# Optimization experiments

Hardware: AMD Instinct MI355X
Metric: run time of the kernel (lower is better)

## Reference

```python
import jax, jax.numpy as jnp
import numpy as np

VOXEL_SIZE = np.array([0.2, 0.2, 4.0], dtype=np.float32)
PC_MIN = np.array([0.0, -40.0, -3.0], dtype=np.float32)
BN_EPS = 1e-3
N_POINTS = 1_500_000
N_VOXELS = 200_000
C_IN = 7   # (4 - 3) + 6 stats channels (cluster offset + voxel-center offset)
C_OUT = 64


def setup_inputs() -> dict:
    key = jax.random.key(0)
    ks = jax.random.split(key, 8)
    features = jax.random.normal(ks[0], (N_POINTS, 4), dtype=jnp.float32)
    point2voxel = jax.random.randint(ks[1], (N_POINTS,), 0, N_VOXELS).astype(jnp.int32)
    voxel_coors = jnp.stack([
        jax.random.randint(ks[2], (N_VOXELS,), 0, 2),    # batch idx
        jnp.zeros((N_VOXELS,), jnp.int32),               # z (pillars -> 0)
        jax.random.randint(ks[3], (N_VOXELS,), 0, 400),  # y bin
        jax.random.randint(ks[4], (N_VOXELS,), 0, 352),  # x bin
    ], axis=1).astype(jnp.int32)
    W = jax.random.normal(ks[5], (C_IN, C_OUT), dtype=jnp.float32) * 0.1
    bn_gamma = jnp.ones((C_OUT,), jnp.float32)
    bn_beta = jnp.zeros((C_OUT,), jnp.float32)
    bn_mean = jax.random.normal(ks[6], (C_OUT,), dtype=jnp.float32) * 0.01
    bn_var = jax.random.uniform(ks[7], (C_OUT,), minval=0.5, maxval=1.5, dtype=jnp.float32)
    return dict(features=features, W=W, bn_gamma=bn_gamma, bn_beta=bn_beta,
                bn_mean=bn_mean, bn_var=bn_var, point2voxel=point2voxel,
                voxel_coors=voxel_coors)


def reference(features, W, bn_gamma, bn_beta, bn_mean, bn_var, point2voxel, voxel_coors):
    M = voxel_coors.shape[0]
    xyz = features[:, :3]

    # --- stats: cluster-center offset (per-voxel mean of xyz, mapped back) ---
    cnt = jax.ops.segment_sum(jnp.ones((xyz.shape[0],), xyz.dtype), point2voxel,
                              num_segments=M)
    vmean = jax.ops.segment_sum(xyz, point2voxel, num_segments=M)
    vmean = vmean / jnp.maximum(cnt, 1.0)[:, None]
    cluster_off = xyz - vmean[point2voxel]

    # --- stats: voxel-center offset ---
    vs = jnp.asarray(VOXEL_SIZE)
    mn = jnp.asarray(PC_MIN)
    # coors layout is (batch, z, y, x) -> take (x, y, z)
    centers = (voxel_coors[:, jnp.array([3, 2, 1])].astype(jnp.float32) + 0.5) * vs + mn
    center_off = xyz - centers[point2voxel]

    feats = jnp.concatenate([cluster_off, center_off, features[:, 3:]], axis=-1)  # [N,7]

    # --- PFN layer: Linear(bias=False) + BN1d (eval stats) + ReLU ---
    h = feats @ W
    h = (h - bn_mean) * jax.lax.rsqrt(bn_var + BN_EPS) * bn_gamma + bn_beta
    h = jax.nn.relu(h)

    # --- scatter max-reduce to voxels ---
    vfeats = jax.ops.segment_max(h, point2voxel, num_segments=M)
    vfeats = jnp.where(jnp.isfinite(vfeats), vfeats, 0.0)  # guard rare empty voxels
    return vfeats, voxel_coors
```

## Files before the change

### kernel.cpp

```cpp
#include <hip/hip_runtime.h>


#define BBITS  7
#define BVOX   (1 << BBITS)
#define PCAP   1280
#define NR     (PCAP / 256)
#define NBBITS 7
#define NBLK   (1 << NBBITS)
#define BMAX   1600
#define SCH    4096

__global__ __launch_bounds__(256) void hist_k(const int* __restrict__ p2v,
                                              int* __restrict__ mat,
                                              int N, int NB, int chunk) {
    __shared__ int h[BMAX];
    int b = blockIdx.x, tid = threadIdx.x;
    for (int k = tid; k < NB; k += 256) h[k] = 0;
    __syncthreads();
    int s = b * chunk, e = min(N, s + chunk);
    for (int i = s + tid; i < e; i += 256)
        atomicAdd(&h[p2v[i] >> BBITS], 1);
    __syncthreads();
    for (int k = tid; k < NB; k += 256) mat[b * NB + k] = h[k];
}

__global__ void scanA_k(int* __restrict__ mat, int* __restrict__ bsum,
                        int NB, int S) {
    __shared__ int s[256];
    int tid = threadIdx.x;
    int base = blockIdx.x * SCH + tid * 16;
    int idx[16], c[16];
    int tsum = 0;
#pragma unroll
    for (int j = 0; j < 16; ++j) {
        int p = base + j;
        if (p < S) {
            int k = p >> NBBITS, b = p & (NBLK - 1);
            idx[j] = b * NB + k;
            c[j] = mat[idx[j]];
        } else {
            idx[j] = -1;
            c[j] = 0;
        }
        tsum += c[j];
    }
    s[tid] = tsum;
    __syncthreads();
    for (int off = 1; off < 256; off <<= 1) {
        int v = (tid >= off) ? s[tid - off] : 0;
        __syncthreads();
        s[tid] += v;
        __syncthreads();
    }
    int run = s[tid] - tsum;
#pragma unroll
    for (int j = 0; j < 16; ++j) {
        if (idx[j] >= 0) mat[idx[j]] = run;
        run += c[j];
    }
    if (tid == 255) bsum[blockIdx.x] = s[255];
}

__global__ void scanB_k(int* __restrict__ bsum, int nb) {
    __shared__ int s[256];
    int tid = threadIdx.x;
    int v = (tid < nb) ? bsum[tid] : 0;
    s[tid] = v;
    __syncthreads();
    for (int off = 1; off < 256; off <<= 1) {
        int t = (tid >= off) ? s[tid - off] : 0;
        __syncthreads();
        s[tid] += t;
        __syncthreads();
    }
    if (tid < nb) bsum[tid] = s[tid] - v;
}

__global__ __launch_bounds__(256) void scatter_pay_k(
    const int* __restrict__ p2v, const float4* __restrict__ feats,
    const int* __restrict__ mat, const int* __restrict__ bsum,
    float4* __restrict__ pay, unsigned char* __restrict__ voxid,
    int N, int NB, int chunk) {
    __shared__ int cur[BMAX];
    int b = blockIdx.x, tid = threadIdx.x;
    for (int k = tid; k < NB; k += 256)
        cur[k] = mat[b * NB + k] + bsum[((k << NBBITS) | b) >> 12];
    __syncthreads();
    int s = b * chunk, e = min(N, s + chunk);
    for (int i = s + tid; i < e; i += 256) {
        int v = p2v[i];
        int k = v >> BBITS;
        int pos = atomicAdd(&cur[k], 1);
        pay[pos] = feats[i];
        voxid[pos] = (unsigned char)(v & (BVOX - 1));
    }
}

__global__ __launch_bounds__(256, 4) void gather_bucket_k(
    const float4* __restrict__ pay, const unsigned char* __restrict__ voxid,
    const int* __restrict__ mat, const int* __restrict__ bsum,
    const float* __restrict__ W,
    const float* __restrict__ gamma, const float* __restrict__ beta,
    const float* __restrict__ mean, const float* __restrict__ var,
    const int* __restrict__ coors,
    float* __restrict__ out_v, float* __restrict__ out_c,
    int M, int NB, int N) {
    __shared__ float4 s_pay[PCAP];
    __shared__ int    s_cnt[BVOX];
    __shared__ int    s_off[BVOX];
    __shared__ int    s_cur[BVOX];
    __shared__ float4 s_cen[BVOX];

    int bk = blockIdx.x, tid = threadIdx.x;
    int lane = tid & 63, w = tid >> 6;

    float w0 = W[0 * 64 + lane], w1 = W[1 * 64 + lane], w2 = W[2 * 64 + lane];
    float w3 = W[3 * 64 + lane], w4 = W[4 * 64 + lane], w5 = W[5 * 64 + lane];
    float w6 = W[6 * 64 + lane];
    float sc = gamma[lane] * rsqrtf(var[lane] + 1e-3f);
    float bi = beta[lane] - mean[lane] * sc;
    float sgn = (sc >= 0.0f) ? 1.0f : -1.0f;
    float u0 = sgn * (w0 + w3), u1 = sgn * (w1 + w4);
    float u2 = sgn * (w2 + w5), u3 = sgn * w6;

    int s = mat[bk] + bsum[(bk << NBBITS) >> 12];
    int e = (bk + 1 < NB) ? (mat[bk + 1] + bsum[((bk + 1) << NBBITS) >> 12]) : N;
    int L = min(e - s, PCAP);

    float4 fv[NR];
    int vx[NR];
#pragma unroll
    for (int r = 0; r < NR; ++r) {
        int j = tid + r * 256;
        if (j < L) {
            fv[r] = pay[s + j];
            vx[r] = voxid[s + j];
        } else {
            vx[r] = -1;
        }
    }

    if (tid < BVOX) s_cnt[tid] = 0;
    __syncthreads();
#pragma unroll
    for (int r = 0; r < NR; ++r)
        if (vx[r] >= 0) atomicAdd(&s_cnt[vx[r]], 1);

    int vbase = bk << BBITS;
    if (tid < BVOX) {
        int vg = vbase + tid;
        if (vg < M) {
            int4 cc = ((const int4*)coors)[vg];
            ((float4*)out_c)[vg] = make_float4((float)cc.x, (float)cc.y,
                                               (float)cc.z, (float)cc.w);
            s_cen[tid] = make_float4((cc.w + 0.5f) * 0.2f,
                                     (cc.z + 0.5f) * 0.2f - 40.0f,
                                     (cc.y + 0.5f) * 4.0f - 3.0f, 0.0f);
        }
    }
    __syncthreads();

    if (w == 0) {
        int c0 = s_cnt[2 * lane], c1 = s_cnt[2 * lane + 1];
        int cp = c0 + c1;
        int x = cp;
        for (int off = 1; off < 64; off <<= 1) {
            int t = __shfl_up(x, off);
            if (lane >= off) x += t;
        }
        int ex = x - cp;
        s_off[2 * lane] = ex;
        s_off[2 * lane + 1] = ex + c0;
        s_cur[2 * lane] = ex;
        s_cur[2 * lane + 1] = ex + c0;
    }
    __syncthreads();

#pragma unroll
    for (int r = 0; r < NR; ++r)
        if (vx[r] >= 0) {
            int pos = atomicAdd(&s_cur[vx[r]], 1);
            s_pay[pos] = fv[r];
        }
    __syncthreads();

    int lv0 = w << 5;
    int cnts[32];
#pragma unroll
    for (int q = 0; q < 32; ++q) cnts[q] = s_cnt[lv0 + q];
    int st = s_off[lv0];

#pragma unroll
    for (int q = 0; q < 32; ++q) {
        int lv = lv0 + q;
        int v = vbase + lv;
        int npts = cnts[q];
        float4 cen = s_cen[lv];
        float sx = 0.f, sy = 0.f, sz = 0.f;
        float amax = -3.402823466e+38f;
        int i = 0;
        for (; i + 3 < npts; i += 4) {
            float4 f0 = s_pay[st + i + 0];
            float4 f1 = s_pay[st + i + 1];
            float4 f2 = s_pay[st + i + 2];
            float4 f3 = s_pay[st + i + 3];
            sx += f0.x + f1.x + f2.x + f3.x;
            sy += f0.y + f1.y + f2.y + f3.y;
            sz += f0.z + f1.z + f2.z + f3.z;
            float a0 = f0.x * u0 + f0.y * u1 + f0.z * u2 + f0.w * u3;
            float a1 = f1.x * u0 + f1.y * u1 + f1.z * u2 + f1.w * u3;
            float a2 = f2.x * u0 + f2.y * u1 + f2.z * u2 + f2.w * u3;
            float a3 = f3.x * u0 + f3.y * u1 + f3.z * u2 + f3.w * u3;
            amax = fmaxf(fmaxf(fmaxf(amax, a0), fmaxf(a1, a2)), a3);
        }
        for (; i < npts; ++i) {
            float4 f = s_pay[st + i];
            sx += f.x; sy += f.y; sz += f.z;
            float a = f.x * u0 + f.y * u1 + f.z * u2 + f.w * u3;
            amax = fmaxf(amax, a);
        }
        float res = 0.0f;
        if (npts > 0) {
            float inv = 1.0f / (float)npts;
            float mx = sx * inv, my = sy * inv, mz = sz * inv;
            float K = mx * w0 + my * w1 + mz * w2 +
                      cen.x * w3 + cen.y * w4 + cen.z * w5;
            float aext = sgn * amax;
            res = fmaxf((aext - K) * sc + bi, 0.0f);
        }
        if (v < M) out_v[(size_t)v * 64 + lane] = res;
        st += npts;
    }
}

extern "C" void kernel_launch(void* const* d_in, const int* in_sizes, int n_in,
                              void* d_out, int out_size, void* d_ws, size_t ws_size,
                              hipStream_t stream) {
    const float* features = (const float*)d_in[0];
    const float* W        = (const float*)d_in[1];
    const float* gamma    = (const float*)d_in[2];
    const float* beta     = (const float*)d_in[3];
    const float* mean     = (const float*)d_in[4];
    const float* var      = (const float*)d_in[5];
    const int*   p2v      = (const int*)d_in[6];
    const int*   coors    = (const int*)d_in[7];
    int N = in_sizes[0] / 4;
    int M = in_sizes[7] / 4;

    int NB = (M + BVOX - 1) >> BBITS;
    int S = NB * NBLK;
    int chunk = (N + NBLK - 1) / NBLK;

    float4* pay           = (float4*)d_ws;
    unsigned char* voxid  = (unsigned char*)(pay + N);
    int* mat              = (int*)(voxid + ((N + 3) & ~3));
    int* bsum             = mat + S;

    float* out_v = (float*)d_out;
    float* out_c = out_v + (size_t)M * 64;

    hist_k<<<NBLK, 256, 0, stream>>>(p2v, mat, N, NB, chunk);
    int nbA = (S + SCH - 1) / SCH;
    scanA_k<<<nbA, 256, 0, stream>>>(mat, bsum, NB, S);
    scanB_k<<<1, 256, 0, stream>>>(bsum, nbA);
    scatter_pay_k<<<NBLK, 256, 0, stream>>>(
        p2v, (const float4*)features, mat, bsum, pay, voxid, N, NB, chunk);
    gather_bucket_k<<<NB, 256, 0, stream>>>(
        pay, voxid, mat, bsum, W, gamma, beta, mean, var,
        coors, out_v, out_c, M, NB, N);
}
```

Baseline: 135.5 us.

## Double voxel bucket size and accumulate per-voxel xyz sums with LDS atomics

Bucket width grows from 128 to 256 voxels, so the gather kernel launches half as many blocks, each with 512 threads and a 2560-point shared payload. The scatter kernel also moves to 512 threads per block. Per-voxel xyz sums are now built with shared-memory float atomics while the payload is loaded, which takes the summation out of the per-voxel max loop. The intent is to cut per-block overhead and shorten the inner loop. In exchange there is more LDS atomic contention, float summation order becomes nondeterministic, and buckets holding more than 2560 points would be truncated.

```diff
diff --git a/kernel.cpp b/kernel.cpp
--- a/kernel.cpp
+++ b/kernel.cpp
@@ -1,31 +1,32 @@
 #include <hip/hip_runtime.h>
 
 
-#define BBITS  7
+#define BBITS  8
 #define BVOX   (1 << BBITS)
-#define PCAP   1280
-#define NR     (PCAP / 256)
+#define PCAP   2560
+#define GT     512
+#define NR     (PCAP / GT)
 #define NBBITS 7
 #define NBLK   (1 << NBBITS)
-#define BMAX   1600
+#define BMAX   800
 #define SCH    4096
 
 __global__ __launch_bounds__(256) void hist_k(const int* __restrict__ p2v,
                                               int* __restrict__ mat,
-                                              int N, int NB, int chunk) {
+                                              int N, int NBIN, int chunk) {
     __shared__ int h[BMAX];
     int b = blockIdx.x, tid = threadIdx.x;
-    for (int k = tid; k < NB; k += 256) h[k] = 0;
+    for (int k = tid; k < NBIN; k += 256) h[k] = 0;
     __syncthreads();
     int s = b * chunk, e = min(N, s + chunk);
     for (int i = s + tid; i < e; i += 256)
         atomicAdd(&h[p2v[i] >> BBITS], 1);
     __syncthreads();
-    for (int k = tid; k < NB; k += 256) mat[b * NB + k] = h[k];
+    for (int k = tid; k < NBIN; k += 256) mat[b * NBIN + k] = h[k];
 }
 
 __global__ void scanA_k(int* __restrict__ mat, int* __restrict__ bsum,
-                        int NB, int S) {
+                        int NBIN, int S) {
     __shared__ int s[256];
     int tid = threadIdx.x;
     int base = blockIdx.x * SCH + tid * 16;
@@ -35,8 +36,8 @@
     for (int j = 0; j < 16; ++j) {
         int p = base + j;
         if (p < S) {
-            int k = p >> NBBITS, b = p & (NBLK - 1);
-            idx[j] = b * NB + k;
+            int g = p >> NBBITS, b = p & (NBLK - 1);
+            idx[j] = b * NBIN + g;
             c[j] = mat[idx[j]];
         } else {
             idx[j] = -1;
@@ -76,27 +77,27 @@
     if (tid < nb) bsum[tid] = s[tid] - v;
 }
 
-__global__ __launch_bounds__(256) void scatter_pay_k(
+__global__ __launch_bounds__(512) void scatter_pay_k(
     const int* __restrict__ p2v, const float4* __restrict__ feats,
     const int* __restrict__ mat, const int* __restrict__ bsum,
     float4* __restrict__ pay, unsigned char* __restrict__ voxid,
-    int N, int NB, int chunk) {
+    int N, int NBIN, int chunk) {
     __shared__ int cur[BMAX];
     int b = blockIdx.x, tid = threadIdx.x;
-    for (int k = tid; k < NB; k += 256)
-        cur[k] = mat[b * NB + k] + bsum[((k << NBBITS) | b) >> 12];
+    for (int g = tid; g < NBIN; g += 512)
+        cur[g] = mat[b * NBIN + g] + bsum[((g << NBBITS) | b) >> 12];
     __syncthreads();
     int s = b * chunk, e = min(N, s + chunk);
-    for (int i = s + tid; i < e; i += 256) {
+    for (int i = s + tid; i < e; i += 512) {
         int v = p2v[i];
-        int k = v >> BBITS;
-        int pos = atomicAdd(&cur[k], 1);
+        int g = v >> BBITS;
+        int pos = atomicAdd(&cur[g], 1);
         pay[pos] = feats[i];
         voxid[pos] = (unsigned char)(v & (BVOX - 1));
     }
 }
 
-__global__ __launch_bounds__(256, 4) void gather_bucket_k(
+__global__ __launch_bounds__(512, 4) void gather_bucket_k(
     const float4* __restrict__ pay, const unsigned char* __restrict__ voxid,
     const int* __restrict__ mat, const int* __restrict__ bsum,
     const float* __restrict__ W,
@@ -104,8 +105,9 @@
     const float* __restrict__ mean, const float* __restrict__ var,
     const int* __restrict__ coors,
     float* __restrict__ out_v, float* __restrict__ out_c,
-    int M, int NB, int N) {
+    int M, int NBIN, int N) {
     __shared__ float4 s_pay[PCAP];
+    __shared__ float  s_sx[BVOX], s_sy[BVOX], s_sz[BVOX];
     __shared__ int    s_cnt[BVOX];
     __shared__ int    s_off[BVOX];
     __shared__ int    s_cur[BVOX];
@@ -124,14 +126,14 @@
     float u2 = sgn * (w2 + w5), u3 = sgn * w6;
 
     int s = mat[bk] + bsum[(bk << NBBITS) >> 12];
-    int e = (bk + 1 < NB) ? (mat[bk + 1] + bsum[((bk + 1) << NBBITS) >> 12]) : N;
+    int e = (bk + 1 < NBIN) ? (mat[bk + 1] + bsum[((bk + 1) << NBBITS) >> 12]) : N;
     int L = min(e - s, PCAP);
 
     float4 fv[NR];
     int vx[NR];
 #pragma unroll
     for (int r = 0; r < NR; ++r) {
-        int j = tid + r * 256;
+        int j = tid + r * GT;
         if (j < L) {
             fv[r] = pay[s + j];
             vx[r] = voxid[s + j];
@@ -140,11 +142,19 @@
         }
     }
 
-    if (tid < BVOX) s_cnt[tid] = 0;
+    if (tid < BVOX) {
+        s_cnt[tid] = 0;
+        s_sx[tid] = 0.f; s_sy[tid] = 0.f; s_sz[tid] = 0.f;
+    }
     __syncthreads();
 #pragma unroll
     for (int r = 0; r < NR; ++r)
-        if (vx[r] >= 0) atomicAdd(&s_cnt[vx[r]], 1);
+        if (vx[r] >= 0) {
+            atomicAdd(&s_cnt[vx[r]], 1);
+            atomicAdd(&s_sx[vx[r]], fv[r].x);
+            atomicAdd(&s_sy[vx[r]], fv[r].y);
+            atomicAdd(&s_sz[vx[r]], fv[r].z);
+        }
 
     int vbase = bk << BBITS;
     if (tid < BVOX) {
@@ -161,18 +171,23 @@
     __syncthreads();
 
     if (w == 0) {
-        int c0 = s_cnt[2 * lane], c1 = s_cnt[2 * lane + 1];
-        int cp = c0 + c1;
-        int x = cp;
+        int c0 = s_cnt[4 * lane + 0], c1 = s_cnt[4 * lane + 1];
+        int c2 = s_cnt[4 * lane + 2], c3 = s_cnt[4 * lane + 3];
+        int t = c0 + c1 + c2 + c3;
+        int x = t;
         for (int off = 1; off < 64; off <<= 1) {
-            int t = __shfl_up(x, off);
-            if (lane >= off) x += t;
-        }
-        int ex = x - cp;
-        s_off[2 * lane] = ex;
-        s_off[2 * lane + 1] = ex + c0;
-        s_cur[2 * lane] = ex;
-        s_cur[2 * lane + 1] = ex + c0;
+            int y = __shfl_up(x, off);
+            if (lane >= off) x += y;
+        }
+        int ex = x - t;
+        s_off[4 * lane + 0] = ex;
+        s_off[4 * lane + 1] = ex + c0;
+        s_off[4 * lane + 2] = ex + c0 + c1;
+        s_off[4 * lane + 3] = ex + c0 + c1 + c2;
+        s_cur[4 * lane + 0] = ex;
+        s_cur[4 * lane + 1] = ex + c0;
+        s_cur[4 * lane + 2] = ex + c0 + c1;
+        s_cur[4 * lane + 3] = ex + c0 + c1 + c2;
     }
     __syncthreads();
 
@@ -196,7 +211,6 @@
         int v = vbase + lv;
         int npts = cnts[q];
         float4 cen = s_cen[lv];
-        float sx = 0.f, sy = 0.f, sz = 0.f;
         float amax = -3.402823466e+38f;
         int i = 0;
         for (; i + 3 < npts; i += 4) {
@@ -204,9 +218,6 @@
             float4 f1 = s_pay[st + i + 1];
             float4 f2 = s_pay[st + i + 2];
             float4 f3 = s_pay[st + i + 3];
-            sx += f0.x + f1.x + f2.x + f3.x;
-            sy += f0.y + f1.y + f2.y + f3.y;
-            sz += f0.z + f1.z + f2.z + f3.z;
             float a0 = f0.x * u0 + f0.y * u1 + f0.z * u2 + f0.w * u3;
             float a1 = f1.x * u0 + f1.y * u1 + f1.z * u2 + f1.w * u3;
             float a2 = f2.x * u0 + f2.y * u1 + f2.z * u2 + f2.w * u3;
@@ -215,14 +226,13 @@
         }
         for (; i < npts; ++i) {
             float4 f = s_pay[st + i];
-            sx += f.x; sy += f.y; sz += f.z;
             float a = f.x * u0 + f.y * u1 + f.z * u2 + f.w * u3;
             amax = fmaxf(amax, a);
         }
         float res = 0.0f;
         if (npts > 0) {
             float inv = 1.0f / (float)npts;
-            float mx = sx * inv, my = sy * inv, mz = sz * inv;
+            float mx = s_sx[lv] * inv, my = s_sy[lv] * inv, mz = s_sz[lv] * inv;
             float K = mx * w0 + my * w1 + mz * w2 +
                       cen.x * w3 + cen.y * w4 + cen.z * w5;
             float aext = sgn * amax;
@@ -247,8 +257,8 @@
     int N = in_sizes[0] / 4;
     int M = in_sizes[7] / 4;
 
-    int NB = (M + BVOX - 1) >> BBITS;
-    int S = NB * NBLK;
+    int NBIN = (M + BVOX - 1) >> BBITS;
+    int S = NBIN * NBLK;
     int chunk = (N + NBLK - 1) / NBLK;
 
     float4* pay           = (float4*)d_ws;
@@ -259,13 +269,13 @@
     float* out_v = (float*)d_out;
     float* out_c = out_v + (size_t)M * 64;
 
-    hist_k<<<NBLK, 256, 0, stream>>>(p2v, mat, N, NB, chunk);
+    hist_k<<<NBLK, 256, 0, stream>>>(p2v, mat, N, NBIN, chunk);
     int nbA = (S + SCH - 1) / SCH;
-    scanA_k<<<nbA, 256, 0, stream>>>(mat, bsum, NB, S);
+    scanA_k<<<nbA, 256, 0, stream>>>(mat, bsum, NBIN, S);
     scanB_k<<<1, 256, 0, stream>>>(bsum, nbA);
-    scatter_pay_k<<<NBLK, 256, 0, stream>>>(
-        p2v, (const float4*)features, mat, bsum, pay, voxid, N, NB, chunk);
-    gather_bucket_k<<<NB, 256, 0, stream>>>(
+    scatter_pay_k<<<NBLK, 512, 0, stream>>>(
+        p2v, (const float4*)features, mat, bsum, pay, voxid, N, NBIN, chunk);
+    gather_bucket_k<<<NBIN, GT, 0, stream>>>(
         pay, voxid, mat, bsum, W, gamma, beta, mean, var,
-        coors, out_v, out_c, M, NB, N);
-}
+        coors, out_v, out_c, M, NBIN, N);
+}
```

Measured after the change: 147.4 us. 8.8% more time.
